# Optimization experiments

Hardware: AMD Instinct MI355X
Metric: run time of the kernel (lower is better)

Reference implementation:

```python
import jax, jax.numpy as jnp
import numpy as np
from jax import lax

EPS = 1e-6
BLOCK_SIZE = 64


def _feature_map(x, W):
    # x: (B,H,N,S,D), W: (H,D,F) -> (B,H,N,S,2F), computed in fp32
    u = jnp.einsum('bhnsd,hdf->bhnsf', x, W).astype(jnp.float32)
    return jnp.concatenate([jax.nn.softmax(u, axis=-1), jax.nn.softmax(-u, axis=-1)], axis=-1)


def setup_inputs() -> dict:
    key = jax.random.key(0)
    k1, k2, k3, k4, k5 = jax.random.split(key, 5)
    B, H, L, D, F = 2, 16, 4096, 64, 64
    q = jax.random.normal(k1, (B, H, L, D), dtype=jnp.float32)
    k = jax.random.normal(k2, (B, H, L, D), dtype=jnp.float32)
    v = jax.random.normal(k3, (B, H, L, D), dtype=jnp.float32)
    # hedgehog_weights initialized as eye(D,F) per head, perturbed so the test is non-trivial
    W = jnp.eye(D, F, dtype=jnp.float32)[None].repeat(H, axis=0) + 0.02 * jax.random.normal(k4, (H, D, F), dtype=jnp.float32)
    alpha = 0.1 * jax.random.normal(k5, (1, H, 1, 1), dtype=jnp.float32)
    return {"query_states": q, "key_states": k, "value_states": v,
            "hedgehog_weights": W, "alpha": alpha}


def _forward(q, k, v, W, alpha):
    B, H, L, D = q.shape
    S = BLOCK_SIZE
    N = L // S  # L chosen divisible by block size (no padding path)
    scaling = D ** (-0.5)
    F2 = 2 * W.shape[-1]

    qb = q.reshape(B, H, N, S, D)
    kb = k.reshape(B, H, N, S, D)
    vb = v.reshape(B, H, N, S, D)
    phi_q = _feature_map(qb, W)  # (B,H,N,S,2F) fp32
    phi_k = _feature_map(kb, W)
    w = jax.nn.sigmoid(alpha)    # (1,H,1,1)

    def step(carry, xs):
        S_state, Z_state = carry            # (B,H,2F,D), (B,H,2F)
        qn, kn, vn, pqn, pkn = xs           # per-block slices
        # linear-attention branch (pre-update state = clean history)
        lin_num = jnp.einsum('bhsf,bhfd->bhsd', pqn, S_state)
        lin_den = jnp.maximum(jnp.einsum('bhsf,bhf->bhs', pqn, Z_state)[..., None], EPS)
        # intra-block softmax branch (unnormalized, shared denominator)
        scores = jnp.einsum('bhsd,bhtd->bhst', qn, kn) * scaling
        a = jnp.exp(scores - scores.max(axis=-1, keepdims=True))
        sm_num = jnp.einsum('bhst,bhtd->bhsd', a, vn)
        sm_den = jnp.maximum(a.sum(axis=-1, keepdims=True), EPS)
        out = (w * sm_num + lin_num) / jnp.maximum(w * sm_den + lin_den, EPS)
        # state update with this block's keys/values
        S_state = S_state + jnp.einsum('bhsf,bhsd->bhfd', pkn, vn)
        Z_state = Z_state + pkn.sum(axis=-2)
        return (S_state, Z_state), out

    init = (jnp.zeros((B, H, F2, D), jnp.float32), jnp.zeros((B, H, F2), jnp.float32))
    xs = (jnp.moveaxis(qb, 2, 0), jnp.moveaxis(kb, 2, 0), jnp.moveaxis(vb, 2, 0),
          jnp.moveaxis(phi_q, 2, 0), jnp.moveaxis(phi_k, 2, 0))
    _, outs = lax.scan(step, init, xs)       # (N,B,H,S,D)
    return jnp.moveaxis(outs, 0, 2).reshape(B, H, L, D)


def reference(query_states, key_states, value_states, hedgehog_weights, alpha):
    return _forward(query_states, key_states, value_states, hedgehog_weights, alpha)
```

## Files before the change

kernel.cpp:

```cpp
#include <hip/hip_runtime.h>
#include <hip/hip_bf16.h>
#include <math.h>

constexpr int Hc = 16, Lc = 4096, Dc = 64;
constexpr int F2 = 128;
constexpr int NBLK = 2048;
constexpr float EPSf = 1e-6f;
constexpr float SCALE = 0.125f;

typedef short short8 __attribute__((ext_vector_type(8)));
typedef float f32x4 __attribute__((ext_vector_type(4)));
typedef unsigned short ushort;
typedef unsigned int uint;
typedef ushort ushort4v __attribute__((ext_vector_type(4)));

__device__ inline ushort f2bf(float x) {
    return __builtin_bit_cast(ushort, __float2bfloat16(x));
}
__device__ inline float bf2f(ushort h) {
    return __builtin_bit_cast(float, ((unsigned)h) << 16);
}
__device__ inline f32x4 zero4() { f32x4 z = {0.f, 0.f, 0.f, 0.f}; return z; }

__device__ inline f32x4 mfma(short8 a, short8 b, f32x4 c) {
    return __builtin_amdgcn_mfma_f32_16x16x32_bf16(a, b, c, 0, 0, 0);
}

__device__ inline void dma16(const void* g, void* l) {
    __builtin_amdgcn_global_load_lds(
        (const __attribute__((address_space(1))) unsigned int*)g,
        (__attribute__((address_space(3))) unsigned int*)l, 16, 0, 0);
}

__device__ inline short8 ldfrag(const char* L, int row, int chunk, int rowbytes, int mask) {
    return *(const short8*)(L + row * rowbytes + ((chunk * 16) ^ ((row & mask) << 4)));
}

__device__ inline short8 gfrag_f32(const float* __restrict__ base, int row, int chunk) {
    const float4* p = (const float4*)(base + row * 64 + chunk * 8);
    float4 a = p[0], b = p[1];
    short8 r;
    r[0] = (short)f2bf(a.x); r[1] = (short)f2bf(a.y); r[2] = (short)f2bf(a.z); r[3] = (short)f2bf(a.w);
    r[4] = (short)f2bf(b.x); r[5] = (short)f2bf(b.y); r[6] = (short)f2bf(b.z); r[7] = (short)f2bf(b.w);
    return r;
}
__device__ inline short8 gfrag_bf16(const ushort* __restrict__ base, int row, int chunk, int rowlen) {
    return *(const short8*)(base + row * rowlen + chunk * 8);
}

__device__ inline void stage_rm(const float* __restrict__ src, char* dst, int t) {
    #pragma unroll
    for (int i = 0; i < 4; ++i) {
        int e = t + i * 256;
        float4 x = ((const float4*)src)[e];
        int r = e >> 4;
        int c4 = (e & 15) * 4;
        ushort4v hv;
        hv[0] = f2bf(x.x); hv[1] = f2bf(x.y); hv[2] = f2bf(x.z); hv[3] = f2bf(x.w);
        *(ushort4v*)(dst + r * 128 + ((c4 * 2) ^ ((r & 7) << 4))) = hv;
    }
}

__device__ inline void stage_tr(const float* __restrict__ src, char* dst, int t) {
    int j = t & 63, g = t >> 6;
    #pragma unroll
    for (int i = 0; i < 4; ++i) {
        int i0 = g * 4 + i * 16;
        ushort4v hv;
        #pragma unroll
        for (int jj = 0; jj < 4; ++jj) hv[jj] = f2bf(src[(i0 + jj) * 64 + j]);
        *(ushort4v*)(dst + j * 128 + ((2 * i0) ^ ((j & 7) << 4))) = hv;
    }
}

__global__ __launch_bounds__(256) void passW(const float* __restrict__ W,
                                             ushort* __restrict__ Wt)
{
    const int h = blockIdx.x, t = threadIdx.x;
    const int f = t & 63, g = t >> 6;
    const float* src = W + (long)h * 4096;
    ushort* dst = Wt + (long)h * 4096;
    #pragma unroll
    for (int i = 0; i < 16; ++i) {
        int d = g * 16 + i;
        dst[f * 64 + d] = f2bf(src[d * 64 + f]);
    }
}

__global__ __launch_bounds__(256) void passA(const float* __restrict__ K,
                                             const float* __restrict__ V,
                                             const ushort* __restrict__ Wt,
                                             ushort* __restrict__ wsS,
                                             float* __restrict__ wsZ,
                                             char* __restrict__ wsV)
{
    __shared__ __align__(16) char lds[26624];
    char* vT = lds;
    char* pT = lds + 8192;
    float* Zp = (float*)(lds + 24576);

    const int t = threadIdx.x, wv = t >> 6, l = t & 63, lr = l & 15, lg = l >> 4;
    const int bid = blockIdx.x, bh = bid >> 6, h = bh & (Hc - 1);
    const long base = (long)bh * (Lc * Dc) + (long)(bid & 63) * (64 * Dc);

    stage_tr(V + base, vT, t);

    const float* kp = K + base;
    const ushort* wt = Wt + (long)h * 4096;

    short8 ak0 = gfrag_f32(kp, 16 * wv + lr, lg);
    short8 ak1 = gfrag_f32(kp, 16 * wv + lr, 4 + lg);
    f32x4 u0[4];
    #pragma unroll
    for (int tf = 0; tf < 4; ++tf) u0[tf] = zero4();
    #pragma unroll
    for (int tf = 0; tf < 4; ++tf) {
        u0[tf] = mfma(ak0, gfrag_bf16(wt, tf * 16 + lr, lg, 64), u0[tf]);
        u0[tf] = mfma(ak1, gfrag_bf16(wt, tf * 16 + lr, 4 + lg, 64), u0[tf]);
    }

    float pp[4][4], pn[4][4];
    float zpa[4] = {0.f,0.f,0.f,0.f}, zna[4] = {0.f,0.f,0.f,0.f};
    #pragma unroll
    for (int r = 0; r < 4; ++r) {
        float sp = 0.f, sn = 0.f;
        #pragma unroll
        for (int tf = 0; tf < 4; ++tf) {
            pp[tf][r] = __expf(u0[tf][r]);  sp += pp[tf][r];
            pn[tf][r] = __expf(-u0[tf][r]); sn += pn[tf][r];
        }
        #pragma unroll
        for (int m = 1; m < 16; m <<= 1) { sp += __shfl_xor(sp, m, 16); sn += __shfl_xor(sn, m, 16); }
        float rp = 1.f / sp, rn = 1.f / sn;
        #pragma unroll
        for (int tf = 0; tf < 4; ++tf) {
            pp[tf][r] *= rp; pn[tf][r] *= rn;
            zpa[tf] += pp[tf][r]; zna[tf] += pn[tf][r];
        }
    }

    const int s0 = 16 * wv + lg * 4;
    #pragma unroll
    for (int tf = 0; tf < 4; ++tf) {
        int f = tf * 16 + lr;
        ushort4v hp, hn;
        #pragma unroll
        for (int r = 0; r < 4; ++r) { hp[r] = f2bf(pp[tf][r]); hn[r] = f2bf(pn[tf][r]); }
        *(ushort4v*)(pT + f * 128 + ((2 * s0) ^ ((f & 7) << 4))) = hp;
        int fn = 64 + f;
        *(ushort4v*)(pT + fn * 128 + ((2 * s0) ^ ((fn & 7) << 4))) = hn;
    }
    #pragma unroll
    for (int tf = 0; tf < 4; ++tf) {
        zpa[tf] += __shfl_xor(zpa[tf], 16); zpa[tf] += __shfl_xor(zpa[tf], 32);
        zna[tf] += __shfl_xor(zna[tf], 16); zna[tf] += __shfl_xor(zna[tf], 32);
    }
    if (l < 16) {
        #pragma unroll
        for (int tf = 0; tf < 4; ++tf) {
            Zp[wv * 128 + tf * 16 + lr]      = zpa[tf];
            Zp[wv * 128 + 64 + tf * 16 + lr] = zna[tf];
        }
    }
    __syncthreads();

    {
        const short8* vs = (const short8*)vT;
        short8* vd = (short8*)(wsV + (long)bid * 8192);
        vd[t]       = vs[t];
        vd[t + 256] = vs[t + 256];
    }

    short8 av0 = ldfrag(vT, 16 * wv + lr, lg, 128, 7);
    short8 av1 = ldfrag(vT, 16 * wv + lr, 4 + lg, 128, 7);
    f32x4 acc[8];
    #pragma unroll
    for (int tf = 0; tf < 8; ++tf) acc[tf] = zero4();
    #pragma unroll
    for (int tf = 0; tf < 8; ++tf) {
        acc[tf] = mfma(av0, ldfrag(pT, tf * 16 + lr, lg, 128, 7), acc[tf]);
        acc[tf] = mfma(av1, ldfrag(pT, tf * 16 + lr, 4 + lg, 128, 7), acc[tf]);
    }
    ushort* o = wsS + (long)bid * (F2 * Dc);
    #pragma unroll
    for (int tf = 0; tf < 8; ++tf)
        #pragma unroll
        for (int r = 0; r < 4; ++r) {
            int d = 16 * wv + lg * 4 + r;
            o[d * 128 + tf * 16 + lr] = f2bf(acc[tf][r]);
        }

    if (t < 128)
        wsZ[(long)bid * F2 + t] = Zp[t] + Zp[128 + t] + Zp[256 + t] + Zp[384 + t];
}

__global__ __launch_bounds__(256) void passB(ushort* __restrict__ wsS,
                                             float* __restrict__ wsZ)
{
    const int t = threadIdx.x;
    if (blockIdx.x >= 256) {
        const int bh = blockIdx.x - 256;
        if (t < 128) {
            float zc = 0.f, zb[32];
            #pragma unroll
            for (int h2 = 0; h2 < 2; ++h2) {
                float* zp = wsZ + ((long)bh * 64 + h2 * 32) * 128 + t;
                #pragma unroll
                for (int i = 0; i < 32; ++i) zb[i] = zp[i * 128];
                #pragma unroll
                for (int i = 0; i < 32; ++i) { float x = zb[i]; zp[i * 128] = zc; zc += x; }
            }
        }
        return;
    }
    const int bh = blockIdx.x >> 3, chunk = blockIdx.x & 7;
    ushort* p = wsS + (long)bh * 64 * 8192 + chunk * 1024 + t * 4;
    float c0 = 0.f, c1 = 0.f, c2 = 0.f, c3 = 0.f;
    ushort4v buf[32];
    #pragma unroll
    for (int h2 = 0; h2 < 2; ++h2) {
        ushort4v* pp = (ushort4v*)(p + (long)h2 * 32 * 8192);
        #pragma unroll
        for (int i = 0; i < 32; ++i) buf[i] = pp[i * 2048];
        #pragma unroll
        for (int i = 0; i < 32; ++i) {
            ushort4v x = buf[i];
            ushort4v cc;
            cc[0] = f2bf(c0); cc[1] = f2bf(c1); cc[2] = f2bf(c2); cc[3] = f2bf(c3);
            pp[i * 2048] = cc;
            c0 += bf2f(x[0]); c1 += bf2f(x[1]); c2 += bf2f(x[2]); c3 += bf2f(x[3]);
        }
    }
}

__global__ __launch_bounds__(256, 3) void passC(const float* __restrict__ Q,
                                                const float* __restrict__ K,
                                                const ushort* __restrict__ Wt,
                                                const float* __restrict__ Alpha,
                                                const ushort* __restrict__ wsS,
                                                const float* __restrict__ wsZ,
                                                const char* __restrict__ wsV,
                                                float* __restrict__ Out)
{
    __shared__ __align__(16) char lds[49152];
    char* vT    = lds;
    char* St    = lds + 8192;
    char* phiAB = lds + 24576;
    char* aAB   = lds + 40960;

    const int t = threadIdx.x, wv = t >> 6, l = t & 63, lr = l & 15, lg = l >> 4;
    const int bid = blockIdx.x, bh = bid >> 6, h = bh & (Hc - 1);
    const long base = (long)bh * (Lc * Dc) + (long)(bid & 63) * (64 * Dc);
    const int s = 16 * wv + lr;

    {
        const char* vg = wsV + (long)bid * 8192;
        #pragma unroll
        for (int i = 0; i < 2; ++i) {
            int jb = wv * 128 + i * 64;
            dma16(vg + (long)(jb + l) * 16, vT + jb * 16);
        }
        const char* sg = (const char*)(wsS + (long)bid * 8192);
        #pragma unroll
        for (int i = 0; i < 4; ++i) {
            int jb = wv * 256 + i * 64;
            int j = jb + l;
            int srcc = (j & ~15) | ((j & 15) ^ ((j >> 4) & 15));
            dma16(sg + (long)srcc * 16, St + jb * 16);
        }
    }

    const float* qp = Q + base;
    short8 bq0 = gfrag_f32(qp, s, lg);
    short8 bq1 = gfrag_f32(qp, s, 4 + lg);
    const ushort* wt = Wt + (long)h * 4096;
    short8 aw[4][2];
    #pragma unroll
    for (int tf = 0; tf < 4; ++tf) {
        aw[tf][0] = gfrag_bf16(wt, tf * 16 + lr, lg, 64);
        aw[tf][1] = gfrag_bf16(wt, tf * 16 + lr, 4 + lg, 64);
    }

    f32x4 uq[4];
    #pragma unroll
    for (int tf = 0; tf < 4; ++tf) uq[tf] = zero4();
    #pragma unroll
    for (int tf = 0; tf < 4; ++tf) {
        uq[tf] = mfma(aw[tf][0], bq0, uq[tf]);
        uq[tf] = mfma(aw[tf][1], bq1, uq[tf]);
    }

    const float* kp = K + base;
    short8 akf[4][2];
    #pragma unroll
    for (int tt = 0; tt < 4; ++tt) {
        akf[tt][0] = gfrag_f32(kp, tt * 16 + lr, lg);
        akf[tt][1] = gfrag_f32(kp, tt * 16 + lr, 4 + lg);
    }

    float sp = 0.f, sn = 0.f;
    float pqp[4][4], pqn[4][4];
    #pragma unroll
    for (int tf = 0; tf < 4; ++tf)
        #pragma unroll
        for (int r = 0; r < 4; ++r) {
            pqp[tf][r] = __expf(uq[tf][r]);  sp += pqp[tf][r];
            pqn[tf][r] = __expf(-uq[tf][r]); sn += pqn[tf][r];
        }
    sp += __shfl_xor(sp, 16); sp += __shfl_xor(sp, 32);
    sn += __shfl_xor(sn, 16); sn += __shfl_xor(sn, 32);
    ushort4v phk[4], phkn[4];
    {
        float rp = 1.f / sp, rn = 1.f / sn;
        #pragma unroll
        for (int tf = 0; tf < 4; ++tf)
            #pragma unroll
            for (int r = 0; r < 4; ++r) {
                phk[tf][r]  = f2bf(pqp[tf][r] * rp);
                phkn[tf][r] = f2bf(pqn[tf][r] * rn);
            }
    }
    const float w = 1.f / (1.f + __expf(-Alpha[h]));

    f32x4 sc[4];
    #pragma unroll
    for (int tt = 0; tt < 4; ++tt) sc[tt] = zero4();
    #pragma unroll
    for (int tt = 0; tt < 4; ++tt) {
        sc[tt] = mfma(akf[tt][0], bq0, sc[tt]);
        sc[tt] = mfma(akf[tt][1], bq1, sc[tt]);
    }
    #pragma unroll
    for (int tt = 0; tt < 4; ++tt)
        #pragma unroll
        for (int r = 0; r < 4; ++r) sc[tt][r] *= SCALE;
    float m2;
    {
        float m01 = fmaxf(fmaxf(fmaxf(sc[0][0], sc[0][1]), fmaxf(sc[0][2], sc[0][3])),
                          fmaxf(fmaxf(sc[1][0], sc[1][1]), fmaxf(sc[1][2], sc[1][3])));
        float m23 = fmaxf(fmaxf(fmaxf(sc[2][0], sc[2][1]), fmaxf(sc[2][2], sc[2][3])),
                          fmaxf(fmaxf(sc[3][0], sc[3][1]), fmaxf(sc[3][2], sc[3][3])));
        m2 = fmaxf(m01, m23);
        m2 = fmaxf(m2, __shfl_xor(m2, 16));
        m2 = fmaxf(m2, __shfl_xor(m2, 32));
    }
    float as = 0.f;
    ushort4v apk[4];
    #pragma unroll
    for (int tt = 0; tt < 4; ++tt)
        #pragma unroll
        for (int r = 0; r < 4; ++r) {
            float e = __expf(sc[tt][r] - m2);
            as += e;
            apk[tt][r] = f2bf(w * e);
        }
    as += __shfl_xor(as, 16); as += __shfl_xor(as, 32);
    const float sden = fmaxf(as, EPSf);

    float zd = 0.f;
    {
        const float* zp = wsZ + (long)bid * 128;
        #pragma unroll
        for (int tf = 0; tf < 4; ++tf) {
            float4 zv = *(const float4*)(zp + tf * 16 + lg * 4);
            float4 zn = *(const float4*)(zp + 64 + tf * 16 + lg * 4);
            #pragma unroll
            for (int r = 0; r < 4; ++r)
                zd += bf2f(phk[tf][r]) * (&zv.x)[r] + bf2f(phkn[tf][r]) * (&zn.x)[r];
        }
    }
    zd += __shfl_xor(zd, 16); zd += __shfl_xor(zd, 32);
    const float lden = fmaxf(zd, EPSf);
    const float inv = 1.f / fmaxf(w * sden + lden, EPSf);

    #pragma unroll
    for (int tt = 0; tt < 4; ++tt)
        *(ushort4v*)(aAB + s * 128 + ((32 * tt + 8 * lg) ^ ((s & 7) << 4))) = apk[tt];
    #pragma unroll
    for (int tf = 0; tf < 4; ++tf) {
        *(ushort4v*)(phiAB + s * 256 + ((32 * tf + 8 * lg) ^ ((s & 15) << 4))) = phk[tf];
        *(ushort4v*)(phiAB + s * 256 + ((128 + 32 * tf + 8 * lg) ^ ((s & 15) << 4))) = phkn[tf];
    }

    __syncthreads();

    f32x4 oacc[4];
    #pragma unroll
    for (int td = 0; td < 4; ++td) oacc[td] = zero4();
    short8 aa0 = ldfrag(aAB, s, lg, 128, 7);
    short8 aa1 = ldfrag(aAB, s, 4 + lg, 128, 7);
    #pragma unroll
    for (int td = 0; td < 4; ++td) {
        oacc[td] = mfma(aa0, ldfrag(vT, td * 16 + lr, lg, 128, 7), oacc[td]);
        oacc[td] = mfma(aa1, ldfrag(vT, td * 16 + lr, 4 + lg, 128, 7), oacc[td]);
    }
    short8 pf[4];
    #pragma unroll
    for (int kc = 0; kc < 4; ++kc) pf[kc] = ldfrag(phiAB, s, kc * 4 + lg, 256, 15);
    #pragma unroll
    for (int td = 0; td < 4; ++td)
        #pragma unroll
        for (int kc = 0; kc < 4; ++kc)
            oacc[td] = mfma(pf[kc], ldfrag(St, td * 16 + lr, kc * 4 + lg, 256, 15), oacc[td]);

    float* op = Out + base;
    #pragma unroll
    for (int r = 0; r < 4; ++r) {
        float invr = __shfl(inv, lg * 4 + r, 16);
        int sr = 16 * wv + lg * 4 + r;
        #pragma unroll
        for (int td = 0; td < 4; ++td)
            op[sr * 64 + td * 16 + lr] = oacc[td][r] * invr;
    }
}

extern "C" void kernel_launch(void* const* d_in, const int* in_sizes, int n_in,
                              void* d_out, int out_size, void* d_ws, size_t ws_size,
                              hipStream_t stream)
{
    const float* q     = (const float*)d_in[0];
    const float* k     = (const float*)d_in[1];
    const float* v     = (const float*)d_in[2];
    const float* W     = (const float*)d_in[3];
    const float* alpha = (const float*)d_in[4];
    float* out = (float*)d_out;

    ushort* wsSb = (ushort*)d_ws;
    float*  wsZ  = (float*)((char*)d_ws + (size_t)NBLK * F2 * Dc * 2);
    ushort* Wtb  = (ushort*)((char*)wsZ + (size_t)NBLK * F2 * 4);
    char*   wsV  = (char*)Wtb + (size_t)Hc * 4096 * 2;

    passW<<<Hc, 256, 0, stream>>>(W, Wtb);
    passA<<<NBLK, 256, 0, stream>>>(k, v, Wtb, wsSb, wsZ, wsV);
    passB<<<288, 256, 0, stream>>>(wsSb, wsZ);
    passC<<<NBLK, 256, 0, stream>>>(q, k, Wtb, alpha, wsSb, wsZ, wsV, out);
}
```

Measured before the change: 81.14 us.

## Stage K through LDS in passC and widen passB prefix-scan parallelism

passC now loads the K block into LDS with a row-major staging helper and reads the MFMA fragments from shared memory, instead of gathering strided fp32 fragments straight from global memory. The phi buffer reuses the K staging region, with an extra barrier to keep them apart, and the Z-denominator computation moves earlier to overlap with the staging. The occupancy hint of 3 is dropped from passC. passB splits the state prefix-scan across twice as many blocks, each thread handling packed bf16 pairs over all 64 blocks with deeper load batching, so more memory parallelism is exposed.

```diff
diff --git a/kernel.cpp b/kernel.cpp
--- a/kernel.cpp
+++ b/kernel.cpp
@@ -194,12 +194,12 @@
         wsZ[(long)bid * F2 + t] = Zp[t] + Zp[128 + t] + Zp[256 + t] + Zp[384 + t];
 }
 
-__global__ __launch_bounds__(256) void passB(ushort* __restrict__ wsS,
+__global__ __launch_bounds__(256) void passB(uint* __restrict__ wsSu,
                                              float* __restrict__ wsZ)
 {
     const int t = threadIdx.x;
-    if (blockIdx.x >= 256) {
-        const int bh = blockIdx.x - 256;
+    if (blockIdx.x >= 512) {
+        const int bh = blockIdx.x - 512;
         if (t < 128) {
             float zc = 0.f, zb[32];
             #pragma unroll
@@ -213,39 +213,38 @@
         }
         return;
     }
-    const int bh = blockIdx.x >> 3, chunk = blockIdx.x & 7;
-    ushort* p = wsS + (long)bh * 64 * 8192 + chunk * 1024 + t * 4;
-    float c0 = 0.f, c1 = 0.f, c2 = 0.f, c3 = 0.f;
-    ushort4v buf[32];
-    #pragma unroll
-    for (int h2 = 0; h2 < 2; ++h2) {
-        ushort4v* pp = (ushort4v*)(p + (long)h2 * 32 * 8192);
-        #pragma unroll
-        for (int i = 0; i < 32; ++i) buf[i] = pp[i * 2048];
-        #pragma unroll
-        for (int i = 0; i < 32; ++i) {
-            ushort4v x = buf[i];
-            ushort4v cc;
-            cc[0] = f2bf(c0); cc[1] = f2bf(c1); cc[2] = f2bf(c2); cc[3] = f2bf(c3);
-            pp[i * 2048] = cc;
-            c0 += bf2f(x[0]); c1 += bf2f(x[1]); c2 += bf2f(x[2]); c3 += bf2f(x[3]);
-        }
-    }
-}
-
-__global__ __launch_bounds__(256, 3) void passC(const float* __restrict__ Q,
-                                                const float* __restrict__ K,
-                                                const ushort* __restrict__ Wt,
-                                                const float* __restrict__ Alpha,
-                                                const ushort* __restrict__ wsS,
-                                                const float* __restrict__ wsZ,
-                                                const char* __restrict__ wsV,
-                                                float* __restrict__ Out)
+    const int bh = blockIdx.x >> 4;
+    const int slice = (blockIdx.x & 15) * 4 + (t >> 6);
+    const int lane = t & 63;
+    uint* p = wsSu + (long)bh * 64 * 4096 + slice * 64 + lane;
+    uint buf[64];
+    #pragma unroll
+    for (int i = 0; i < 64; ++i) buf[i] = p[i * 4096];
+    float c0 = 0.f, c1 = 0.f;
+    #pragma unroll
+    for (int i = 0; i < 64; ++i) {
+        uint x = buf[i];
+        uint pc = ((uint)f2bf(c1) << 16) | (uint)f2bf(c0);
+        p[i * 4096] = pc;
+        c0 += bf2f((ushort)(x & 0xffffu));
+        c1 += bf2f((ushort)(x >> 16));
+    }
+}
+
+__global__ __launch_bounds__(256) void passC(const float* __restrict__ Q,
+                                             const float* __restrict__ K,
+                                             const ushort* __restrict__ Wt,
+                                             const float* __restrict__ Alpha,
+                                             const ushort* __restrict__ wsS,
+                                             const float* __restrict__ wsZ,
+                                             const char* __restrict__ wsV,
+                                             float* __restrict__ Out)
 {
     __shared__ __align__(16) char lds[49152];
-    char* vT    = lds;
-    char* St    = lds + 8192;
-    char* phiAB = lds + 24576;
+    char* kR    = lds;
+    char* phiAB = lds;
+    char* vT    = lds + 16384;
+    char* St    = lds + 24576;
     char* aAB   = lds + 40960;
 
     const int t = threadIdx.x, wv = t >> 6, l = t & 63, lr = l & 15, lg = l >> 4;
@@ -281,6 +280,8 @@
         aw[tf][1] = gfrag_bf16(wt, tf * 16 + lr, 4 + lg, 64);
     }
 
+    stage_rm(K + base, kR, t);
+
     f32x4 uq[4];
     #pragma unroll
     for (int tf = 0; tf < 4; ++tf) uq[tf] = zero4();
@@ -288,14 +289,6 @@
     for (int tf = 0; tf < 4; ++tf) {
         uq[tf] = mfma(aw[tf][0], bq0, uq[tf]);
         uq[tf] = mfma(aw[tf][1], bq1, uq[tf]);
-    }
-
-    const float* kp = K + base;
-    short8 akf[4][2];
-    #pragma unroll
-    for (int tt = 0; tt < 4; ++tt) {
-        akf[tt][0] = gfrag_f32(kp, tt * 16 + lr, lg);
-        akf[tt][1] = gfrag_f32(kp, tt * 16 + lr, 4 + lg);
     }
 
     float sp = 0.f, sn = 0.f;
@@ -322,13 +315,30 @@
     }
     const float w = 1.f / (1.f + __expf(-Alpha[h]));
 
+    float zd = 0.f;
+    {
+        const float* zp = wsZ + (long)bid * 128;
+        #pragma unroll
+        for (int tf = 0; tf < 4; ++tf) {
+            float4 zv = *(const float4*)(zp + tf * 16 + lg * 4);
+            float4 zn = *(const float4*)(zp + 64 + tf * 16 + lg * 4);
+            #pragma unroll
+            for (int r = 0; r < 4; ++r)
+                zd += bf2f(phk[tf][r]) * (&zv.x)[r] + bf2f(phkn[tf][r]) * (&zn.x)[r];
+        }
+    }
+    zd += __shfl_xor(zd, 16); zd += __shfl_xor(zd, 32);
+    const float lden = fmaxf(zd, EPSf);
+
+    __syncthreads();
+
     f32x4 sc[4];
     #pragma unroll
     for (int tt = 0; tt < 4; ++tt) sc[tt] = zero4();
     #pragma unroll
     for (int tt = 0; tt < 4; ++tt) {
-        sc[tt] = mfma(akf[tt][0], bq0, sc[tt]);
-        sc[tt] = mfma(akf[tt][1], bq1, sc[tt]);
+        sc[tt] = mfma(ldfrag(kR, tt * 16 + lr, lg, 128, 7), bq0, sc[tt]);
+        sc[tt] = mfma(ldfrag(kR, tt * 16 + lr, 4 + lg, 128, 7), bq1, sc[tt]);
     }
     #pragma unroll
     for (int tt = 0; tt < 4; ++tt)
@@ -356,33 +366,19 @@
         }
     as += __shfl_xor(as, 16); as += __shfl_xor(as, 32);
     const float sden = fmaxf(as, EPSf);
-
-    float zd = 0.f;
-    {
-        const float* zp = wsZ + (long)bid * 128;
-        #pragma unroll
-        for (int tf = 0; tf < 4; ++tf) {
-            float4 zv = *(const float4*)(zp + tf * 16 + lg * 4);
-            float4 zn = *(const float4*)(zp + 64 + tf * 16 + lg * 4);
-            #pragma unroll
-            for (int r = 0; r < 4; ++r)
-                zd += bf2f(phk[tf][r]) * (&zv.x)[r] + bf2f(phkn[tf][r]) * (&zn.x)[r];
-        }
-    }
-    zd += __shfl_xor(zd, 16); zd += __shfl_xor(zd, 32);
-    const float lden = fmaxf(zd, EPSf);
     const float inv = 1.f / fmaxf(w * sden + lden, EPSf);
 
     #pragma unroll
     for (int tt = 0; tt < 4; ++tt)
         *(ushort4v*)(aAB + s * 128 + ((32 * tt + 8 * lg) ^ ((s & 7) << 4))) = apk[tt];
+
+    __syncthreads();
+
     #pragma unroll
     for (int tf = 0; tf < 4; ++tf) {
         *(ushort4v*)(phiAB + s * 256 + ((32 * tf + 8 * lg) ^ ((s & 15) << 4))) = phk[tf];
         *(ushort4v*)(phiAB + s * 256 + ((128 + 32 * tf + 8 * lg) ^ ((s & 15) << 4))) = phkn[tf];
     }
-
-    __syncthreads();
 
     f32x4 oacc[4];
     #pragma unroll
@@ -432,6 +428,6 @@
 
     passW<<<Hc, 256, 0, stream>>>(W, Wtb);
     passA<<<NBLK, 256, 0, stream>>>(k, v, Wtb, wsSb, wsZ, wsV);
-    passB<<<288, 256, 0, stream>>>(wsSb, wsZ);
+    passB<<<544, 256, 0, stream>>>((uint*)wsSb, wsZ);
     passC<<<NBLK, 256, 0, stream>>>(q, k, Wtb, alpha, wsSb, wsZ, wsV, out);
 }
```

After: 72.90 us. 1.11x faster.
